# Kernel tuning notes

Measured on AMD Instinct MI355X. Metric: run time of the kernel, lower is better.

## Reference

```python
import jax, jax.numpy as jnp
import numpy as np

B, S, H = 2, 2048, 1024
NUM_HEAD = 16
HEAD = H // NUM_HEAD
NEG = -10000000000.0


def setup_inputs() -> dict:
    key = jax.random.key(0)
    ks = jax.random.split(key, 10)
    scale = 1.0 / np.sqrt(H)
    return {
        "query": jax.random.normal(ks[0], (B, S, H), jnp.float32),
        "key": jax.random.normal(ks[1], (B, S, H), jnp.float32),
        "value": jax.random.normal(ks[2], (B, S, H), jnp.float32),
        "mask": jax.random.randint(ks[3], (B, S), 0, 2, jnp.int32),
        "Wq": jax.random.normal(ks[4], (H, H), jnp.float32) * scale,
        "bq": jnp.zeros((H,), jnp.float32),
        "Wk": jax.random.normal(ks[5], (H, H), jnp.float32) * scale,
        "bk": jnp.zeros((H,), jnp.float32),
        "Wv": jax.random.normal(ks[6], (H, H), jnp.float32) * scale,
        "bv": jnp.zeros((H,), jnp.float32),
    }


def reference(query, key, value, mask, Wq, bq, Wk, bk, Wv, bv):
    b, s, h = query.shape
    # Linear projections (torch Linear: x @ W.T + b), split into heads -> [b, nh, s, hd]
    def proj(x, W, bias):
        y = x @ W.T + bias
        return y.reshape(b, s, NUM_HEAD, HEAD).transpose(0, 2, 1, 3)

    q = proj(query, Wq, bq)
    k = proj(key, Wk, bk)
    v = proj(value, Wv, bv)

    # NOTE: original module has NO 1/sqrt(head_dim) scaling -- faithful.
    attn_score = jnp.einsum("bhqd,bhkd->bhqk", q, k)  # [b, nh, s, s]
    # key-padding mask bias: 0 where mask==1, -1e10 where mask==0, broadcast over query dim
    bias_add = jnp.where(mask[:, None, None, :] == 0, NEG, 0.0).astype(attn_score.dtype)
    attn_score = attn_score + bias_add
    attn_ratio = jax.nn.softmax(attn_score, axis=-1)
    out = jnp.einsum("bhqk,bhkd->bhqd", attn_ratio, v)  # [b, nh, s, hd]
    out = out.transpose(0, 2, 1, 3).reshape(b, s, h)
    # Dropout is identity in eval mode; output_linear is defined but never used in forward.
    return out
```

## Files before the change

### kernel.cpp

```cpp
#include <hip/hip_runtime.h>

#define BATCH 2
#define S_LEN 2048
#define HDIM  1024
#define NHEAD 16
#define HD    64
#define NEGBIAS -1e10f

typedef __attribute__((ext_vector_type(8))) _Float16 half8;
typedef __attribute__((ext_vector_type(4))) _Float16 half4;
typedef __attribute__((ext_vector_type(4))) float   f32x4;

__global__ __launch_bounds__(256) void proj_gemm_f16(
    const float* __restrict__ Xq, const float* __restrict__ Wq, const float* __restrict__ bq,
    const float* __restrict__ Xk, const float* __restrict__ Wk, const float* __restrict__ bk,
    const float* __restrict__ Xv, const float* __restrict__ Wv, const float* __restrict__ bv,
    _Float16* __restrict__ Qb, _Float16* __restrict__ Kb, _Float16* __restrict__ Vtb)
{
    const int z = blockIdx.z;
    const float* X    = (z == 0) ? Xq : (z == 1) ? Xk : Xv;
    const float* W    = (z == 0) ? Wq : (z == 1) ? Wk : Wv;
    const float* bias = (z == 0) ? bq : (z == 1) ? bk : bv;
    _Float16* Y       = (z == 0) ? Qb : (z == 1) ? Kb : Vtb;

    const int n0 = blockIdx.x * 128;
    const int m0 = blockIdx.y * 128;

    __shared__ __align__(16) _Float16 As[128][40];
    __shared__ __align__(16) _Float16 Bs[128][40];

    const int t    = threadIdx.x;
    const int w    = t >> 6;
    const int lane = t & 63;
    const int quad = lane >> 4;
    const int lc   = lane & 15;
    const int wm   = (w >> 1) * 64;
    const int wn   = (w & 1) * 64;

    const f32x4 fzero = {0.f, 0.f, 0.f, 0.f};
    f32x4 acc[4][4];
#pragma unroll
    for (int i = 0; i < 4; i++)
#pragma unroll
        for (int j = 0; j < 4; j++) acc[i][j] = fzero;

    const int srow = t >> 2;
    const int sc   = t & 3;

    float4 xa[2][2], wa[2][2];
#define PROJ_ISSUE(K0)                                                        \
    {                                                                         \
        _Pragma("unroll")                                                     \
        for (int hf = 0; hf < 2; hf++) {                                      \
            const float* gx = X + (size_t)(m0 + srow + hf * 64) * HDIM + (K0) + sc * 8; \
            xa[hf][0] = *(const float4*)gx;                                   \
            xa[hf][1] = *(const float4*)(gx + 4);                             \
            const float* gw = W + (size_t)(n0 + srow + hf * 64) * HDIM + (K0) + sc * 8; \
            wa[hf][0] = *(const float4*)gw;                                   \
            wa[hf][1] = *(const float4*)(gw + 4);                             \
        }                                                                     \
    }

    PROJ_ISSUE(0)

    for (int k0 = 0; k0 < HDIM; k0 += 32) {
        if (k0) __syncthreads();
#pragma unroll
        for (int hf = 0; hf < 2; hf++) {
            int row = srow + hf * 64;
            half8 vx;
            vx[0] = (_Float16)xa[hf][0].x; vx[1] = (_Float16)xa[hf][0].y;
            vx[2] = (_Float16)xa[hf][0].z; vx[3] = (_Float16)xa[hf][0].w;
            vx[4] = (_Float16)xa[hf][1].x; vx[5] = (_Float16)xa[hf][1].y;
            vx[6] = (_Float16)xa[hf][1].z; vx[7] = (_Float16)xa[hf][1].w;
            *(half8*)&As[row][sc * 8] = vx;
            half8 vw;
            vw[0] = (_Float16)wa[hf][0].x; vw[1] = (_Float16)wa[hf][0].y;
            vw[2] = (_Float16)wa[hf][0].z; vw[3] = (_Float16)wa[hf][0].w;
            vw[4] = (_Float16)wa[hf][1].x; vw[5] = (_Float16)wa[hf][1].y;
            vw[6] = (_Float16)wa[hf][1].z; vw[7] = (_Float16)wa[hf][1].w;
            *(half8*)&Bs[row][sc * 8] = vw;
        }
        __syncthreads();

        if (k0 + 32 < HDIM) PROJ_ISSUE(k0 + 32)

        half8 af[4], bf[4];
#pragma unroll
        for (int mt = 0; mt < 4; mt++)
            af[mt] = *(const half8*)&As[wm + mt * 16 + lc][quad * 8];
#pragma unroll
        for (int nt = 0; nt < 4; nt++)
            bf[nt] = *(const half8*)&Bs[wn + nt * 16 + lc][quad * 8];
#pragma unroll
        for (int mt = 0; mt < 4; mt++)
#pragma unroll
            for (int nt = 0; nt < 4; nt++)
                acc[mt][nt] = __builtin_amdgcn_mfma_f32_16x16x32_f16(
                    af[mt], bf[nt], acc[mt][nt], 0, 0, 0);
    }

#pragma unroll
    for (int nt = 0; nt < 4; nt++) {
        const int n = n0 + wn + nt * 16 + lc;
        const float bv_ = bias[n];
        const int h = n >> 6, d = n & 63;
#pragma unroll
        for (int mt = 0; mt < 4; mt++) {
#pragma unroll
            for (int r = 0; r < 4; r++) {
                const int m = m0 + wm + mt * 16 + quad * 4 + r;
                const int b = m >> 11, s = m & (S_LEN - 1);
                const int bh = b * NHEAD + h;
                _Float16 val = (_Float16)(acc[mt][nt][r] + bv_);
                if (z == 2)
                    Y[((size_t)bh * HD + d) * S_LEN + s] = val;
                else
                    Y[((size_t)bh * S_LEN + s) * HD + d] = val;
            }
        }
    }
}

__global__ __launch_bounds__(256) void flash_attn_mfma(
    const _Float16* __restrict__ Qb, const _Float16* __restrict__ Kb,
    const _Float16* __restrict__ Vtb, const int* __restrict__ mask,
    float* __restrict__ out)
{
    const int qt = blockIdx.x & 15;
    const int bh = blockIdx.x >> 4;
    const int b  = bh >> 4;
    const int h  = bh & (NHEAD - 1);

    __shared__ __align__(16) _Float16 Ks [64][72];
    __shared__ __align__(16) _Float16 Vts[64][72];
    __shared__ __align__(16) _Float16 Ps [4][32][72];
    __shared__ float biasS[64];

    const int t    = threadIdx.x;
    const int w    = t >> 6;
    const int lane = t & 63;
    const int quad = lane >> 4;
    const int lc   = lane & 15;

    const _Float16* Kbase = Kb  + (size_t)bh * S_LEN * HD;
    const _Float16* Vbase = Vtb + (size_t)bh * HD * S_LEN;
    const int* mbase = mask + b * S_LEN;

    half8 qf[2][2];
#pragma unroll
    for (int qg = 0; qg < 2; qg++) {
        const int qrow = qt * 128 + w * 32 + qg * 16 + lc;
#pragma unroll
        for (int s = 0; s < 2; s++)
            qf[qg][s] = *(const half8*)(Qb + ((size_t)bh * S_LEN + qrow) * HD
                                        + s * 32 + quad * 8);
    }

    const f32x4 fzero = {0.f, 0.f, 0.f, 0.f};
    f32x4 o[2][4];
#pragma unroll
    for (int qg = 0; qg < 2; qg++)
#pragma unroll
        for (int nt = 0; nt < 4; nt++) o[qg][nt] = fzero;
    float mrun[2] = {-3.0e38f, -3.0e38f};
    float lrun[2] = {0.f, 0.f};

    const int rr0 = t >> 3,          cc0 = (t & 7) * 8;
    const int rr1 = (t + 256) >> 3,  cc1 = (t & 7) * 8;

    half8 kpre[2], vpre[2];
    int   mpre;
#define ATTN_ISSUE(KT)                                                        \
    {                                                                         \
        kpre[0] = *(const half8*)(Kbase + (size_t)((KT) + rr0) * HD + cc0);   \
        kpre[1] = *(const half8*)(Kbase + (size_t)((KT) + rr1) * HD + cc1);   \
        vpre[0] = *(const half8*)(Vbase + (size_t)rr0 * S_LEN + (KT) + cc0);  \
        vpre[1] = *(const half8*)(Vbase + (size_t)rr1 * S_LEN + (KT) + cc1);  \
        mpre    = mbase[(KT) + (t & 63)];                                     \
    }

    ATTN_ISSUE(0)

    for (int kt = 0; kt < S_LEN; kt += 64) {
        if (kt) __syncthreads();
        *(half8*)&Ks [rr0][cc0] = kpre[0];
        *(half8*)&Ks [rr1][cc1] = kpre[1];
        *(half8*)&Vts[rr0][cc0] = vpre[0];
        *(half8*)&Vts[rr1][cc1] = vpre[1];
        if (t < 64) biasS[t] = mpre ? 0.f : NEGBIAS;
        __syncthreads();

        if (kt + 64 < S_LEN) ATTN_ISSUE(kt + 64)

        f32x4 scf[2][4];
#pragma unroll
        for (int qg = 0; qg < 2; qg++)
#pragma unroll
            for (int tt = 0; tt < 4; tt++) scf[qg][tt] = fzero;
#pragma unroll
        for (int s = 0; s < 2; s++) {
#pragma unroll
            for (int tt = 0; tt < 4; tt++) {
                half8 kf = *(const half8*)&Ks[tt * 16 + lc][s * 32 + quad * 8];
                scf[0][tt] = __builtin_amdgcn_mfma_f32_16x16x32_f16(kf, qf[0][s], scf[0][tt], 0, 0, 0);
                scf[1][tt] = __builtin_amdgcn_mfma_f32_16x16x32_f16(kf, qf[1][s], scf[1][tt], 0, 0, 0);
            }
        }

#pragma unroll
        for (int tt = 0; tt < 4; tt++) {
            float4 b4 = *(const float4*)&biasS[tt * 16 + quad * 4];
#pragma unroll
            for (int qg = 0; qg < 2; qg++) {
                scf[qg][tt][0] += b4.x; scf[qg][tt][1] += b4.y;
                scf[qg][tt][2] += b4.z; scf[qg][tt][3] += b4.w;
            }
        }

#pragma unroll
        for (int qg = 0; qg < 2; qg++) {
            float mx = scf[qg][0][0];
#pragma unroll
            for (int tt = 0; tt < 4; tt++)
#pragma unroll
                for (int r = 0; r < 4; r++) mx = fmaxf(mx, scf[qg][tt][r]);
            mx = fmaxf(mx, __shfl_xor(mx, 16));
            mx = fmaxf(mx, __shfl_xor(mx, 32));

            float mn = fmaxf(mrun[qg], mx);
            float al = __expf(mrun[qg] - mn);
            float ls = 0.f;
#pragma unroll
            for (int tt = 0; tt < 4; tt++)
#pragma unroll
                for (int r = 0; r < 4; r++) {
                    float p = __expf(scf[qg][tt][r] - mn);
                    scf[qg][tt][r] = p;
                    ls += p;
                }
            ls += __shfl_xor(ls, 16);
            ls += __shfl_xor(ls, 32);
            lrun[qg] = lrun[qg] * al + ls;
            mrun[qg] = mn;
#pragma unroll
            for (int nt = 0; nt < 4; nt++) {
                o[qg][nt][0] *= al; o[qg][nt][1] *= al;
                o[qg][nt][2] *= al; o[qg][nt][3] *= al;
            }

#pragma unroll
            for (int tt = 0; tt < 4; tt++) {
                half4 pk;
                pk[0] = (_Float16)scf[qg][tt][0]; pk[1] = (_Float16)scf[qg][tt][1];
                pk[2] = (_Float16)scf[qg][tt][2]; pk[3] = (_Float16)scf[qg][tt][3];
                *(half4*)&Ps[w][qg * 16 + lc][tt * 16 + quad * 4] = pk;
            }
        }

#pragma unroll
        for (int s = 0; s < 2; s++) {
            half8 pf0 = *(const half8*)&Ps[w][lc]     [s * 32 + quad * 8];
            half8 pf1 = *(const half8*)&Ps[w][16 + lc][s * 32 + quad * 8];
#pragma unroll
            for (int nt = 0; nt < 4; nt++) {
                half8 vf = *(const half8*)&Vts[nt * 16 + lc][s * 32 + quad * 8];
                o[0][nt] = __builtin_amdgcn_mfma_f32_16x16x32_f16(vf, pf0, o[0][nt], 0, 0, 0);
                o[1][nt] = __builtin_amdgcn_mfma_f32_16x16x32_f16(vf, pf1, o[1][nt], 0, 0, 0);
            }
        }
    }

#pragma unroll
    for (int qg = 0; qg < 2; qg++) {
        const int qrow = qt * 128 + w * 32 + qg * 16 + lc;
        const float inv = 1.f / lrun[qg];
        const size_t rowb = ((size_t)b * S_LEN + qrow) * HDIM + h * HD;
#pragma unroll
        for (int nt = 0; nt < 4; nt++) {
            float4 v;
            v.x = o[qg][nt][0] * inv; v.y = o[qg][nt][1] * inv;
            v.z = o[qg][nt][2] * inv; v.w = o[qg][nt][3] * inv;
            *(float4*)&out[rowb + nt * 16 + quad * 4] = v;
        }
    }
}

extern "C" void kernel_launch(void* const* d_in, const int* in_sizes, int n_in,
                              void* d_out, int out_size, void* d_ws, size_t ws_size,
                              hipStream_t stream) {
    const float* query = (const float*)d_in[0];
    const float* key   = (const float*)d_in[1];
    const float* value = (const float*)d_in[2];
    const int*   mask  = (const int*)  d_in[3];
    const float* Wq    = (const float*)d_in[4];
    const float* bq    = (const float*)d_in[5];
    const float* Wk    = (const float*)d_in[6];
    const float* bk    = (const float*)d_in[7];
    const float* Wv    = (const float*)d_in[8];
    const float* bv    = (const float*)d_in[9];
    float* out = (float*)d_out;

    const size_t nElem = (size_t)BATCH * S_LEN * HDIM;
    if (ws_size < 3 * nElem * sizeof(_Float16)) return;
    _Float16* Qb  = (_Float16*)d_ws;
    _Float16* Kb  = Qb + nElem;
    _Float16* Vtb = Kb + nElem;

    dim3 gproj(HDIM / 128, (BATCH * S_LEN) / 128, 3);
    proj_gemm_f16<<<gproj, 256, 0, stream>>>(query, Wq, bq, key, Wk, bk,
                                             value, Wv, bv, Qb, Kb, Vtb);

    flash_attn_mfma<<<BATCH * NHEAD * (S_LEN / 128), 256, 0, stream>>>(
        Qb, Kb, Vtb, mask, out);
}
```

Baseline: 239.6 us.

## Switch attention to 32x32 MFMA tiles, vectorize projection stores, precompute mask bias

The attention kernel moves from 16x16x32 MFMA with two 16-row query groups per wave to a single 32x32x16 MFMA tile per wave. This halves the per-row softmax reductions and cuts the shuffle count and LDS fragment loads. The projection epilogue swaps MFMA operand order for Q/K so each lane writes a contiguous half4 instead of scalar fp16 stores, and V gets vectorized half4 stores too. The mask is converted to a float bias in a separate small kernel and read directly from global memory in attention. That removes the per-tile LDS bias write but adds a kernel launch and extra workspace.

```diff
diff --git a/kernel.cpp b/kernel.cpp
--- a/kernel.cpp
+++ b/kernel.cpp
@@ -7,9 +7,17 @@
 #define HD    64
 #define NEGBIAS -1e10f
 
-typedef __attribute__((ext_vector_type(8))) _Float16 half8;
-typedef __attribute__((ext_vector_type(4))) _Float16 half4;
-typedef __attribute__((ext_vector_type(4))) float   f32x4;
+typedef __attribute__((ext_vector_type(8)))  _Float16 half8;
+typedef __attribute__((ext_vector_type(4)))  _Float16 half4;
+typedef __attribute__((ext_vector_type(4)))  float    f32x4;
+typedef __attribute__((ext_vector_type(16))) float    f32x16;
+
+__global__ __launch_bounds__(256) void cvt_bias(const int* __restrict__ mask,
+                                                float* __restrict__ biasF)
+{
+    int i = blockIdx.x * 256 + threadIdx.x;
+    biasF[i] = mask[i] ? 0.f : NEGBIAS;
+}
 
 __global__ __launch_bounds__(256) void proj_gemm_f16(
     const float* __restrict__ Xq, const float* __restrict__ Wq, const float* __restrict__ bq,
@@ -92,31 +100,55 @@
 #pragma unroll
         for (int nt = 0; nt < 4; nt++)
             bf[nt] = *(const half8*)&Bs[wn + nt * 16 + lc][quad * 8];
-#pragma unroll
-        for (int mt = 0; mt < 4; mt++)
-#pragma unroll
-            for (int nt = 0; nt < 4; nt++)
-                acc[mt][nt] = __builtin_amdgcn_mfma_f32_16x16x32_f16(
-                    af[mt], bf[nt], acc[mt][nt], 0, 0, 0);
-    }
-
-#pragma unroll
-    for (int nt = 0; nt < 4; nt++) {
-        const int n = n0 + wn + nt * 16 + lc;
-        const float bv_ = bias[n];
-        const int h = n >> 6, d = n & 63;
+        if (z == 2) {
+#pragma unroll
+            for (int mt = 0; mt < 4; mt++)
+#pragma unroll
+                for (int nt = 0; nt < 4; nt++)
+                    acc[mt][nt] = __builtin_amdgcn_mfma_f32_16x16x32_f16(
+                        af[mt], bf[nt], acc[mt][nt], 0, 0, 0);
+        } else {
+#pragma unroll
+            for (int mt = 0; mt < 4; mt++)
+#pragma unroll
+                for (int nt = 0; nt < 4; nt++)
+                    acc[mt][nt] = __builtin_amdgcn_mfma_f32_16x16x32_f16(
+                        bf[nt], af[mt], acc[mt][nt], 0, 0, 0);
+        }
+    }
+
+    if (z == 2) {
+#pragma unroll
+        for (int nt = 0; nt < 4; nt++) {
+            const int n = n0 + wn + nt * 16 + lc;
+            const float bv_ = bias[n];
+            const int h = n >> 6, d = n & 63;
+#pragma unroll
+            for (int mt = 0; mt < 4; mt++) {
+                const int m = m0 + wm + mt * 16 + quad * 4;
+                const int b = m >> 11, s = m & (S_LEN - 1);
+                half4 hv;
+#pragma unroll
+                for (int r = 0; r < 4; r++) hv[r] = (_Float16)(acc[mt][nt][r] + bv_);
+                *(half4*)&Y[(((size_t)b * NHEAD + h) * HD + d) * S_LEN + s] = hv;
+            }
+        }
+    } else {
 #pragma unroll
         for (int mt = 0; mt < 4; mt++) {
-#pragma unroll
-            for (int r = 0; r < 4; r++) {
-                const int m = m0 + wm + mt * 16 + quad * 4 + r;
-                const int b = m >> 11, s = m & (S_LEN - 1);
-                const int bh = b * NHEAD + h;
-                _Float16 val = (_Float16)(acc[mt][nt][r] + bv_);
-                if (z == 2)
-                    Y[((size_t)bh * HD + d) * S_LEN + s] = val;
-                else
-                    Y[((size_t)bh * S_LEN + s) * HD + d] = val;
+            const int m = m0 + wm + mt * 16 + lc;
+            const int b = m >> 11, s = m & (S_LEN - 1);
+#pragma unroll
+            for (int nt = 0; nt < 4; nt++) {
+                const int n = n0 + wn + nt * 16 + quad * 4;
+                const int h = n >> 6, d = n & 63;
+                float4 b4 = *(const float4*)&bias[n];
+                half4 hv;
+                hv[0] = (_Float16)(acc[mt][nt][0] + b4.x);
+                hv[1] = (_Float16)(acc[mt][nt][1] + b4.y);
+                hv[2] = (_Float16)(acc[mt][nt][2] + b4.z);
+                hv[3] = (_Float16)(acc[mt][nt][3] + b4.w);
+                *(half4*)&Y[(((size_t)b * NHEAD + h) * S_LEN + s) * HD + d] = hv;
             }
         }
     }
@@ -124,60 +156,53 @@
 
 __global__ __launch_bounds__(256) void flash_attn_mfma(
     const _Float16* __restrict__ Qb, const _Float16* __restrict__ Kb,
-    const _Float16* __restrict__ Vtb, const int* __restrict__ mask,
+    const _Float16* __restrict__ Vtb, const float* __restrict__ biasF,
     float* __restrict__ out)
 {
     const int qt = blockIdx.x & 15;
     const int bh = blockIdx.x >> 4;
     const int b  = bh >> 4;
-    const int h  = bh & (NHEAD - 1);
+    const int hh = bh & (NHEAD - 1);
 
     __shared__ __align__(16) _Float16 Ks [64][72];
     __shared__ __align__(16) _Float16 Vts[64][72];
     __shared__ __align__(16) _Float16 Ps [4][32][72];
-    __shared__ float biasS[64];
 
     const int t    = threadIdx.x;
     const int w    = t >> 6;
     const int lane = t & 63;
-    const int quad = lane >> 4;
-    const int lc   = lane & 15;
+    const int h    = lane >> 5;
+    const int l5   = lane & 31;
 
     const _Float16* Kbase = Kb  + (size_t)bh * S_LEN * HD;
     const _Float16* Vbase = Vtb + (size_t)bh * HD * S_LEN;
-    const int* mbase = mask + b * S_LEN;
-
-    half8 qf[2][2];
-#pragma unroll
-    for (int qg = 0; qg < 2; qg++) {
-        const int qrow = qt * 128 + w * 32 + qg * 16 + lc;
-#pragma unroll
-        for (int s = 0; s < 2; s++)
-            qf[qg][s] = *(const half8*)(Qb + ((size_t)bh * S_LEN + qrow) * HD
-                                        + s * 32 + quad * 8);
-    }
-
-    const f32x4 fzero = {0.f, 0.f, 0.f, 0.f};
-    f32x4 o[2][4];
-#pragma unroll
-    for (int qg = 0; qg < 2; qg++)
-#pragma unroll
-        for (int nt = 0; nt < 4; nt++) o[qg][nt] = fzero;
-    float mrun[2] = {-3.0e38f, -3.0e38f};
-    float lrun[2] = {0.f, 0.f};
-
-    const int rr0 = t >> 3,          cc0 = (t & 7) * 8;
-    const int rr1 = (t + 256) >> 3,  cc1 = (t & 7) * 8;
+    const float* bbase = biasF + b * S_LEN;
+
+    const int qrow = qt * 128 + w * 32 + l5;
+    half8 qf[4];
+#pragma unroll
+    for (int ks = 0; ks < 4; ks++)
+        qf[ks] = *(const half8*)(Qb + ((size_t)bh * S_LEN + qrow) * HD
+                                 + ks * 16 + h * 8);
+
+    f32x16 o[2];
+#pragma unroll
+    for (int dt = 0; dt < 2; dt++)
+#pragma unroll
+        for (int r = 0; r < 16; r++) o[dt][r] = 0.f;
+    float mrun = -3.0e38f;
+    float lrun = 0.f;
+
+    const int rr0 = t >> 3,       cc0 = (t & 7) * 8;
+    const int rr1 = rr0 + 32,     cc1 = cc0;
 
     half8 kpre[2], vpre[2];
-    int   mpre;
 #define ATTN_ISSUE(KT)                                                        \
     {                                                                         \
         kpre[0] = *(const half8*)(Kbase + (size_t)((KT) + rr0) * HD + cc0);   \
         kpre[1] = *(const half8*)(Kbase + (size_t)((KT) + rr1) * HD + cc1);   \
         vpre[0] = *(const half8*)(Vbase + (size_t)rr0 * S_LEN + (KT) + cc0);  \
         vpre[1] = *(const half8*)(Vbase + (size_t)rr1 * S_LEN + (KT) + cc1);  \
-        mpre    = mbase[(KT) + (t & 63)];                                     \
     }
 
     ATTN_ISSUE(0)
@@ -188,102 +213,93 @@
         *(half8*)&Ks [rr1][cc1] = kpre[1];
         *(half8*)&Vts[rr0][cc0] = vpre[0];
         *(half8*)&Vts[rr1][cc1] = vpre[1];
-        if (t < 64) biasS[t] = mpre ? 0.f : NEGBIAS;
         __syncthreads();
 
         if (kt + 64 < S_LEN) ATTN_ISSUE(kt + 64)
 
-        f32x4 scf[2][4];
-#pragma unroll
-        for (int qg = 0; qg < 2; qg++)
-#pragma unroll
-            for (int tt = 0; tt < 4; tt++) scf[qg][tt] = fzero;
-#pragma unroll
-        for (int s = 0; s < 2; s++) {
-#pragma unroll
-            for (int tt = 0; tt < 4; tt++) {
-                half8 kf = *(const half8*)&Ks[tt * 16 + lc][s * 32 + quad * 8];
-                scf[0][tt] = __builtin_amdgcn_mfma_f32_16x16x32_f16(kf, qf[0][s], scf[0][tt], 0, 0, 0);
-                scf[1][tt] = __builtin_amdgcn_mfma_f32_16x16x32_f16(kf, qf[1][s], scf[1][tt], 0, 0, 0);
-            }
-        }
-
-#pragma unroll
-        for (int tt = 0; tt < 4; tt++) {
-            float4 b4 = *(const float4*)&biasS[tt * 16 + quad * 4];
-#pragma unroll
-            for (int qg = 0; qg < 2; qg++) {
-                scf[qg][tt][0] += b4.x; scf[qg][tt][1] += b4.y;
-                scf[qg][tt][2] += b4.z; scf[qg][tt][3] += b4.w;
-            }
-        }
-
-#pragma unroll
-        for (int qg = 0; qg < 2; qg++) {
-            float mx = scf[qg][0][0];
-#pragma unroll
-            for (int tt = 0; tt < 4; tt++)
-#pragma unroll
-                for (int r = 0; r < 4; r++) mx = fmaxf(mx, scf[qg][tt][r]);
-            mx = fmaxf(mx, __shfl_xor(mx, 16));
-            mx = fmaxf(mx, __shfl_xor(mx, 32));
-
-            float mn = fmaxf(mrun[qg], mx);
-            float al = __expf(mrun[qg] - mn);
-            float ls = 0.f;
-#pragma unroll
-            for (int tt = 0; tt < 4; tt++)
-#pragma unroll
-                for (int r = 0; r < 4; r++) {
-                    float p = __expf(scf[qg][tt][r] - mn);
-                    scf[qg][tt][r] = p;
-                    ls += p;
-                }
-            ls += __shfl_xor(ls, 16);
-            ls += __shfl_xor(ls, 32);
-            lrun[qg] = lrun[qg] * al + ls;
-            mrun[qg] = mn;
-#pragma unroll
-            for (int nt = 0; nt < 4; nt++) {
-                o[qg][nt][0] *= al; o[qg][nt][1] *= al;
-                o[qg][nt][2] *= al; o[qg][nt][3] *= al;
-            }
-
-#pragma unroll
-            for (int tt = 0; tt < 4; tt++) {
+        f32x16 scf[2];
+#pragma unroll
+        for (int tt = 0; tt < 2; tt++)
+#pragma unroll
+            for (int r = 0; r < 16; r++) scf[tt][r] = 0.f;
+#pragma unroll
+        for (int ks = 0; ks < 4; ks++) {
+#pragma unroll
+            for (int tt = 0; tt < 2; tt++) {
+                half8 kf = *(const half8*)&Ks[tt * 32 + l5][ks * 16 + h * 8];
+                scf[tt] = __builtin_amdgcn_mfma_f32_32x32x16_f16(kf, qf[ks], scf[tt], 0, 0, 0);
+            }
+        }
+
+#pragma unroll
+        for (int tt = 0; tt < 2; tt++)
+#pragma unroll
+            for (int g = 0; g < 4; g++) {
+                float4 b4 = *(const float4*)&bbase[kt + tt * 32 + g * 8 + h * 4];
+                scf[tt][g * 4 + 0] += b4.x; scf[tt][g * 4 + 1] += b4.y;
+                scf[tt][g * 4 + 2] += b4.z; scf[tt][g * 4 + 3] += b4.w;
+            }
+
+        float mx = scf[0][0];
+#pragma unroll
+        for (int tt = 0; tt < 2; tt++)
+#pragma unroll
+            for (int r = 0; r < 16; r++) mx = fmaxf(mx, scf[tt][r]);
+        mx = fmaxf(mx, __shfl_xor(mx, 32));
+
+        float mn = fmaxf(mrun, mx);
+        float al = __expf(mrun - mn);
+        float ls = 0.f;
+#pragma unroll
+        for (int tt = 0; tt < 2; tt++)
+#pragma unroll
+            for (int r = 0; r < 16; r++) {
+                float p = __expf(scf[tt][r] - mn);
+                scf[tt][r] = p;
+                ls += p;
+            }
+        ls += __shfl_xor(ls, 32);
+        lrun = lrun * al + ls;
+        mrun = mn;
+#pragma unroll
+        for (int dt = 0; dt < 2; dt++)
+#pragma unroll
+            for (int r = 0; r < 16; r++) o[dt][r] *= al;
+
+#pragma unroll
+        for (int tt = 0; tt < 2; tt++)
+#pragma unroll
+            for (int g = 0; g < 4; g++) {
                 half4 pk;
-                pk[0] = (_Float16)scf[qg][tt][0]; pk[1] = (_Float16)scf[qg][tt][1];
-                pk[2] = (_Float16)scf[qg][tt][2]; pk[3] = (_Float16)scf[qg][tt][3];
-                *(half4*)&Ps[w][qg * 16 + lc][tt * 16 + quad * 4] = pk;
-            }
-        }
-
-#pragma unroll
-        for (int s = 0; s < 2; s++) {
-            half8 pf0 = *(const half8*)&Ps[w][lc]     [s * 32 + quad * 8];
-            half8 pf1 = *(const half8*)&Ps[w][16 + lc][s * 32 + quad * 8];
-#pragma unroll
-            for (int nt = 0; nt < 4; nt++) {
-                half8 vf = *(const half8*)&Vts[nt * 16 + lc][s * 32 + quad * 8];
-                o[0][nt] = __builtin_amdgcn_mfma_f32_16x16x32_f16(vf, pf0, o[0][nt], 0, 0, 0);
-                o[1][nt] = __builtin_amdgcn_mfma_f32_16x16x32_f16(vf, pf1, o[1][nt], 0, 0, 0);
-            }
-        }
-    }
-
-#pragma unroll
-    for (int qg = 0; qg < 2; qg++) {
-        const int qrow = qt * 128 + w * 32 + qg * 16 + lc;
-        const float inv = 1.f / lrun[qg];
-        const size_t rowb = ((size_t)b * S_LEN + qrow) * HDIM + h * HD;
-#pragma unroll
-        for (int nt = 0; nt < 4; nt++) {
+                pk[0] = (_Float16)scf[tt][g * 4 + 0];
+                pk[1] = (_Float16)scf[tt][g * 4 + 1];
+                pk[2] = (_Float16)scf[tt][g * 4 + 2];
+                pk[3] = (_Float16)scf[tt][g * 4 + 3];
+                *(half4*)&Ps[w][l5][tt * 32 + g * 8 + h * 4] = pk;
+            }
+
+#pragma unroll
+        for (int ks = 0; ks < 4; ks++) {
+            half8 pf = *(const half8*)&Ps[w][l5][ks * 16 + h * 8];
+#pragma unroll
+            for (int dt = 0; dt < 2; dt++) {
+                half8 vf = *(const half8*)&Vts[dt * 32 + l5][ks * 16 + h * 8];
+                o[dt] = __builtin_amdgcn_mfma_f32_32x32x16_f16(vf, pf, o[dt], 0, 0, 0);
+            }
+        }
+    }
+
+    const float inv = 1.f / lrun;
+    const size_t rowb = ((size_t)b * S_LEN + qrow) * HDIM + hh * HD;
+#pragma unroll
+    for (int dt = 0; dt < 2; dt++)
+#pragma unroll
+        for (int g = 0; g < 4; g++) {
             float4 v;
-            v.x = o[qg][nt][0] * inv; v.y = o[qg][nt][1] * inv;
-            v.z = o[qg][nt][2] * inv; v.w = o[qg][nt][3] * inv;
-            *(float4*)&out[rowb + nt * 16 + quad * 4] = v;
-        }
-    }
+            v.x = o[dt][g * 4 + 0] * inv; v.y = o[dt][g * 4 + 1] * inv;
+            v.z = o[dt][g * 4 + 2] * inv; v.w = o[dt][g * 4 + 3] * inv;
+            *(float4*)&out[rowb + dt * 32 + g * 8 + h * 4] = v;
+        }
 }
 
 extern "C" void kernel_launch(void* const* d_in, const int* in_sizes, int n_in,
@@ -302,15 +318,20 @@
     float* out = (float*)d_out;
 
     const size_t nElem = (size_t)BATCH * S_LEN * HDIM;
-    if (ws_size < 3 * nElem * sizeof(_Float16)) return;
-    _Float16* Qb  = (_Float16*)d_ws;
-    _Float16* Kb  = Qb + nElem;
-    _Float16* Vtb = Kb + nElem;
+    const size_t need = 3 * nElem * sizeof(_Float16)
+                      + (size_t)BATCH * S_LEN * sizeof(float);
+    if (ws_size < need) return;
+    _Float16* Qb    = (_Float16*)d_ws;
+    _Float16* Kb    = Qb + nElem;
+    _Float16* Vtb   = Kb + nElem;
+    float*    biasF = (float*)(Vtb + nElem);
+
+    cvt_bias<<<(BATCH * S_LEN) / 256, 256, 0, stream>>>(mask, biasF);
 
     dim3 gproj(HDIM / 128, (BATCH * S_LEN) / 128, 3);
     proj_gemm_f16<<<gproj, 256, 0, stream>>>(query, Wq, bq, key, Wk, bk,
                                              value, Wv, bv, Qb, Kb, Vtb);
 
     flash_attn_mfma<<<BATCH * NHEAD * (S_LEN / 128), 256, 0, stream>>>(
-        Qb, Kb, Vtb, mask, out);
+        Qb, Kb, Vtb, biasF, out);
 }
```

After: 265.9 us. 1.11x slower.
